# Optimization experiments

Measured on AMD Instinct MI355X. Metric: run time of the kernel, lower is better.

## Reference

```python
import jax, jax.numpy as jnp
import numpy as np

R, N, F, B = 8, 4096, 256, 16384


def setup_inputs() -> dict:
    key = jax.random.key(0)
    ks = jax.random.split(key, 9)
    adjacency = jax.random.uniform(ks[0], (R, N, N), dtype=jnp.float32)
    features = jax.random.normal(ks[1], (N, F), dtype=jnp.float32)
    c = jax.random.uniform(ks[2], (R, N, 1), dtype=jnp.float32)
    W1 = jax.random.normal(ks[3], (R, F, F), dtype=jnp.float32)
    W2 = jax.random.normal(ks[4], (R, F, F), dtype=jnp.float32)
    # DistMult relation matrices initialized as diagonal matrices (as in torch source)
    rel_mats = jax.vmap(jnp.diag)(jax.random.normal(ks[5], (R, F), dtype=jnp.float32))
    e1_idx = jax.random.randint(ks[6], (B,), 0, N, dtype=jnp.int32)
    rel_idx = jax.random.randint(ks[7], (B,), 0, R, dtype=jnp.int32)
    e2_idx = jax.random.randint(ks[8], (B,), 0, N, dtype=jnp.int32)
    return {"adjacency": adjacency, "features": features, "c": c,
            "W1": W1, "W2": W2, "rel_mats": rel_mats,
            "e1_idx": e1_idx, "rel_idx": rel_idx, "e2_idx": e2_idx}


def _rgcn_layer(A, H, c, W):
    # y = sum_r c[r] * (A[r] @ H @ W[r].T)
    AH = jnp.einsum('rnm,mf->rnf', A, H)          # [R,N,F]
    out = jnp.einsum('rnf,rof->rno', AH, W)       # [R,N,O]
    return jnp.sum(c * out, axis=0)               # [N,O]


def reference(adjacency, features, c, W1, W2, rel_mats, e1_idx, rel_idx, e2_idx):
    H = _rgcn_layer(adjacency, features, c, W1)
    H = _rgcn_layer(adjacency, H, c, W2)
    E1 = H[e1_idx]                                # [B,F]
    E2 = H[e2_idx]                                # [B,F]
    # score_b = sigmoid(E1_b @ M[rel_b] @ E2_b), computed without gathering [B,F,F]
    T = jnp.einsum('bf,rfg->brg', E1, rel_mats)   # [B,R,F]
    Tb = jnp.take_along_axis(T, rel_idx[:, None, None], axis=1)[:, 0]  # [B,F]
    return jax.nn.sigmoid(jnp.sum(Tb * E2, axis=-1))  # [B]
```

## Files before the change

kernel.cpp:

```cpp
#include <hip/hip_runtime.h>
#include <math.h>

#define NN 4096
#define FF 256
#define RR 8
#define BQ 16384

typedef _Float16 half_t;
typedef half_t v8h __attribute__((ext_vector_type(8)));
typedef float  v4f __attribute__((ext_vector_type(4)));

#define G_SCALE     0.015625f
#define G_SCALE_INV 64.0f

__global__ __launch_bounds__(256) void gemm_g(const float* __restrict__ H,
                                              const float* __restrict__ W,
                                              half_t* __restrict__ Ght,
                                              half_t* __restrict__ Glt) {
    __shared__ float smem[2 * 32 * 68];
    float (*Hs)[68] = (float(*)[68])smem;
    float (*Ws)[68] = (float(*)[68])(smem + 2176);

    const int tid = threadIdx.x;
    const int r   = blockIdx.z;
    const int o0  = blockIdx.x * 64;
    const int m0  = blockIdx.y * 64;
    const int tx  = tid & 15;
    const int ty  = tid >> 4;

    const float* __restrict__ Wr = W + (size_t)r * FF * FF;

    const int lr = tid >> 2;
    const int lc = (tid & 3) * 8;

    float acc[4][4];
#pragma unroll
    for (int i = 0; i < 4; ++i)
#pragma unroll
        for (int j = 0; j < 4; ++j) acc[i][j] = 0.0f;

    for (int fb = 0; fb < FF; fb += 32) {
        float4 h0 = *(const float4*)&H[(size_t)(m0 + lr) * FF + fb + lc];
        float4 h1 = *(const float4*)&H[(size_t)(m0 + lr) * FF + fb + lc + 4];
        float4 w0 = *(const float4*)&Wr[(size_t)(o0 + lr) * FF + fb + lc];
        float4 w1 = *(const float4*)&Wr[(size_t)(o0 + lr) * FF + fb + lc + 4];

        __syncthreads();
        Hs[lc + 0][lr] = h0.x;  Hs[lc + 1][lr] = h0.y;
        Hs[lc + 2][lr] = h0.z;  Hs[lc + 3][lr] = h0.w;
        Hs[lc + 4][lr] = h1.x;  Hs[lc + 5][lr] = h1.y;
        Hs[lc + 6][lr] = h1.z;  Hs[lc + 7][lr] = h1.w;
        Ws[lc + 0][lr] = w0.x;  Ws[lc + 1][lr] = w0.y;
        Ws[lc + 2][lr] = w0.z;  Ws[lc + 3][lr] = w0.w;
        Ws[lc + 4][lr] = w1.x;  Ws[lc + 5][lr] = w1.y;
        Ws[lc + 6][lr] = w1.z;  Ws[lc + 7][lr] = w1.w;
        __syncthreads();

#pragma unroll
        for (int k = 0; k < 32; ++k) {
            float4 hv = *(const float4*)&Hs[k][ty * 4];
            float4 wv = *(const float4*)&Ws[k][tx * 4];
            float a[4] = {hv.x, hv.y, hv.z, hv.w};
            float b[4] = {wv.x, wv.y, wv.z, wv.w};
#pragma unroll
            for (int i = 0; i < 4; ++i)
#pragma unroll
                for (int j = 0; j < 4; ++j) acc[i][j] += a[i] * b[j];
        }
    }

    __syncthreads();
    float (*T)[65] = (float(*)[65])smem;
#pragma unroll
    for (int i = 0; i < 4; ++i)
#pragma unroll
        for (int j = 0; j < 4; ++j)
            T[ty * 4 + i][tx * 4 + j] = acc[i][j] * G_SCALE;
    __syncthreads();

    const int fr = tid >> 2;
    const int mc = (tid & 3) << 4;
    v8h h0, h1, l0, l1;
#pragma unroll
    for (int q = 0; q < 8; ++q) {
        float v = T[mc + q][fr];
        half_t hh = (half_t)v;
        h0[q] = hh;
        l0[q] = (half_t)(v - (float)hh);
    }
#pragma unroll
    for (int q = 0; q < 8; ++q) {
        float v = T[mc + 8 + q][fr];
        half_t hh = (half_t)v;
        h1[q] = hh;
        l1[q] = (half_t)(v - (float)hh);
    }
    const size_t off = ((size_t)r * FF + o0 + fr) * NN + m0 + mc;
    *(v8h*)(Ght + off)     = h0;
    *(v8h*)(Ght + off + 8) = h1;
    *(v8h*)(Glt + off)     = l0;
    *(v8h*)(Glt + off + 8) = l1;
}

__global__ __launch_bounds__(256, 2) void gemm_ag(const float* __restrict__ A,
                                                  const half_t* __restrict__ Ght,
                                                  const half_t* __restrict__ Glt,
                                                  const float* __restrict__ c,
                                                  float* __restrict__ P) {
    __shared__ half_t Ah[128][40];
    __shared__ half_t Al[128][40];
    __shared__ half_t Bh[128][40];
    __shared__ half_t Bl[128][40];

    const int tid = threadIdx.x;
    const int r   = blockIdx.z;
    const int f0  = blockIdx.x * 128;
    const int m0  = blockIdx.y * 128;

    const float*  __restrict__ Ar  = A   + (size_t)r * NN * NN;
    const half_t* __restrict__ BhG = Ght + ((size_t)r * FF + f0) * NN;
    const half_t* __restrict__ BlG = Glt + ((size_t)r * FF + f0) * NN;

    const int srow  = tid >> 1;
    const int skoff = (tid & 1) * 16;

    const int wid  = tid >> 6;
    const int lane = tid & 63;
    const int wr   = wid >> 1;
    const int wc   = wid & 1;
    const int lrow = lane & 15;
    const int lk   = (lane >> 4) * 8;

    v4f acc[4][4];
#pragma unroll
    for (int m = 0; m < 4; ++m)
#pragma unroll
        for (int n = 0; n < 4; ++n) acc[m][n] = (v4f){0.f, 0.f, 0.f, 0.f};

    const float*  Arow  = Ar  + (size_t)(m0 + srow) * NN;
    const half_t* Bhrow = BhG + (size_t)srow * NN;
    const half_t* Blrow = BlG + (size_t)srow * NN;

    float4 pa0 = *(const float4*)(Arow + skoff);
    float4 pa1 = *(const float4*)(Arow + skoff + 4);
    float4 pa2 = *(const float4*)(Arow + skoff + 8);
    float4 pa3 = *(const float4*)(Arow + skoff + 12);
    float4 pbh0 = *(const float4*)(Bhrow + skoff);
    float4 pbh1 = *(const float4*)(Bhrow + skoff + 8);
    float4 pbl0 = *(const float4*)(Blrow + skoff);
    float4 pbl1 = *(const float4*)(Blrow + skoff + 8);

    for (int kb = 0; kb < NN; kb += 32) {
        __syncthreads();
        {
            float av[16];
            *(float4*)(av + 0)  = pa0;
            *(float4*)(av + 4)  = pa1;
            *(float4*)(av + 8)  = pa2;
            *(float4*)(av + 12) = pa3;
            v8h h0, h1, l0, l1;
#pragma unroll
            for (int e = 0; e < 8; ++e) {
                half_t hh = (half_t)av[e];
                h0[e] = hh;
                l0[e] = (half_t)(av[e] - (float)hh);
            }
#pragma unroll
            for (int e = 0; e < 8; ++e) {
                half_t hh = (half_t)av[8 + e];
                h1[e] = hh;
                l1[e] = (half_t)(av[8 + e] - (float)hh);
            }
            *(v8h*)&Ah[srow][skoff]     = h0;
            *(v8h*)&Ah[srow][skoff + 8] = h1;
            *(v8h*)&Al[srow][skoff]     = l0;
            *(v8h*)&Al[srow][skoff + 8] = l1;
            *(float4*)&Bh[srow][skoff]     = pbh0;
            *(float4*)&Bh[srow][skoff + 8] = pbh1;
            *(float4*)&Bl[srow][skoff]     = pbl0;
            *(float4*)&Bl[srow][skoff + 8] = pbl1;
        }
        __syncthreads();

        if (kb + 32 < NN) {
            const int kn = kb + 32;
            pa0 = *(const float4*)(Arow + kn + skoff);
            pa1 = *(const float4*)(Arow + kn + skoff + 4);
            pa2 = *(const float4*)(Arow + kn + skoff + 8);
            pa3 = *(const float4*)(Arow + kn + skoff + 12);
            pbh0 = *(const float4*)(Bhrow + kn + skoff);
            pbh1 = *(const float4*)(Bhrow + kn + skoff + 8);
            pbl0 = *(const float4*)(Blrow + kn + skoff);
            pbl1 = *(const float4*)(Blrow + kn + skoff + 8);
        }

        v8h bh[4], bl[4];
#pragma unroll
        for (int n = 0; n < 4; ++n) {
            const int bc = wc * 64 + n * 16 + lrow;
            bh[n] = *(const v8h*)&Bh[bc][lk];
            bl[n] = *(const v8h*)&Bl[bc][lk];
        }
#pragma unroll
        for (int m = 0; m < 4; ++m) {
            const int ar = wr * 64 + m * 16 + lrow;
            v8h ahf = *(const v8h*)&Ah[ar][lk];
            v8h alf = *(const v8h*)&Al[ar][lk];
#pragma unroll
            for (int n = 0; n < 4; ++n) {
                acc[m][n] = __builtin_amdgcn_mfma_f32_16x16x32_f16(alf, bh[n], acc[m][n], 0, 0, 0);
                acc[m][n] = __builtin_amdgcn_mfma_f32_16x16x32_f16(ahf, bl[n], acc[m][n], 0, 0, 0);
                acc[m][n] = __builtin_amdgcn_mfma_f32_16x16x32_f16(ahf, bh[n], acc[m][n], 0, 0, 0);
            }
        }
    }

    float* __restrict__ Pp = P + (size_t)r * NN * FF;
#pragma unroll
    for (int m = 0; m < 4; ++m) {
        const int gm0 = m0 + wr * 64 + m * 16 + ((lane >> 4) << 2);
        float cv[4];
#pragma unroll
        for (int j = 0; j < 4; ++j)
            cv[j] = c[r * NN + gm0 + j] * G_SCALE_INV;
#pragma unroll
        for (int n = 0; n < 4; ++n) {
            const int gf = f0 + wc * 64 + n * 16 + (lane & 15);
#pragma unroll
            for (int j = 0; j < 4; ++j)
                Pp[(size_t)(gm0 + j) * FF + gf] = acc[m][n][j] * cv[j];
        }
    }
}

__global__ __launch_bounds__(256) void reduce_p(const float* __restrict__ P,
                                                float* __restrict__ Hout) {
    const size_t idx = ((size_t)blockIdx.x * 256 + threadIdx.x) * 4;
    float4 s = *(const float4*)&P[idx];
#pragma unroll
    for (int r = 1; r < RR; ++r) {
        float4 v = *(const float4*)&P[(size_t)r * NN * FF + idx];
        s.x += v.x; s.y += v.y; s.z += v.z; s.w += v.w;
    }
    *(float4*)&Hout[idx] = s;
}

__global__ __launch_bounds__(256) void score_k(const float* __restrict__ H2,
                                               const float* __restrict__ relm,
                                               const int* __restrict__ e1,
                                               const int* __restrict__ rel,
                                               const int* __restrict__ e2,
                                               float* __restrict__ out) {
    const int wave = threadIdx.x >> 6;
    const int lane = threadIdx.x & 63;
    const int b = blockIdx.x * 4 + wave;
    if (b >= BQ) return;

    const int rr = rel[b];
    const float4* __restrict__ x = (const float4*)(H2 + (size_t)e1[b] * FF);
    const float4* __restrict__ y = (const float4*)(H2 + (size_t)e2[b] * FF);
    const float* __restrict__ M = relm + (size_t)rr * FF * FF;

    float4 xv = x[lane];
    float4 yv = y[lane];
    const int f = lane * 4;
    float s = xv.x * yv.x * M[(size_t)(f + 0) * (FF + 1)]
            + xv.y * yv.y * M[(size_t)(f + 1) * (FF + 1)]
            + xv.z * yv.z * M[(size_t)(f + 2) * (FF + 1)]
            + xv.w * yv.w * M[(size_t)(f + 3) * (FF + 1)];

#pragma unroll
    for (int off = 32; off > 0; off >>= 1) s += __shfl_down(s, off, 64);

    if (lane == 0) out[b] = 1.0f / (1.0f + expf(-s));
}

extern "C" void kernel_launch(void* const* d_in, const int* in_sizes, int n_in,
                              void* d_out, int out_size, void* d_ws, size_t ws_size,
                              hipStream_t stream) {
    const float* A    = (const float*)d_in[0];
    const float* feat = (const float*)d_in[1];
    const float* c    = (const float*)d_in[2];
    const float* W1   = (const float*)d_in[3];
    const float* W2   = (const float*)d_in[4];
    const float* relm = (const float*)d_in[5];
    const int*   e1   = (const int*)d_in[6];
    const int*   rel  = (const int*)d_in[7];
    const int*   e2   = (const int*)d_in[8];
    float* out = (float*)d_out;

    const size_t GT = (size_t)RR * FF * NN;
    half_t* Ght = (half_t*)d_ws;
    half_t* Glt = Ght + GT;
    float*  P   = (float*)(Glt + GT);
    float*  H   = P + (size_t)RR * NN * FF;

    dim3 gg(FF / 64, NN / 64, RR);
    dim3 ga(FF / 128, NN / 128, RR);
    const int gr = (NN * FF / 4) / 256;

    gemm_g  <<<gg, 256, 0, stream>>>(feat, W1, Ght, Glt);
    gemm_ag <<<ga, 256, 0, stream>>>(A, Ght, Glt, c, P);
    reduce_p<<<gr, 256, 0, stream>>>(P, H);
    gemm_g  <<<gg, 256, 0, stream>>>(H, W2, Ght, Glt);
    gemm_ag <<<ga, 256, 0, stream>>>(A, Ght, Glt, c, P);
    reduce_p<<<gr, 256, 0, stream>>>(P, H);
    score_k<<<BQ / 4, 256, 0, stream>>>(H, relm, e1, rel, e2, out);
}
```

Before: 1.231 ms.

## Pre-split adjacency into fp16 hi/lo once and split-K the aggregation GEMM

```diff
diff --git a/kernel.cpp b/kernel.cpp
--- a/kernel.cpp
+++ b/kernel.cpp
@@ -102,15 +102,141 @@
     *(v8h*)(Glt + off + 8) = l1;
 }
 
+__global__ __launch_bounds__(256) void split_a(const float* __restrict__ A,
+                                               half_t* __restrict__ Ah,
+                                               half_t* __restrict__ Al) {
+    const size_t total  = (size_t)RR * NN * NN / 8;
+    const size_t stride = (size_t)gridDim.x * 256;
+    for (size_t g = (size_t)blockIdx.x * 256 + threadIdx.x; g < total; g += stride) {
+        const float* src = A + g * 8;
+        float4 f0 = *(const float4*)(src);
+        float4 f1 = *(const float4*)(src + 4);
+        float av[8] = {f0.x, f0.y, f0.z, f0.w, f1.x, f1.y, f1.z, f1.w};
+        v8h h, l;
+#pragma unroll
+        for (int e = 0; e < 8; ++e) {
+            half_t hh = (half_t)av[e];
+            h[e] = hh;
+            l[e] = (half_t)(av[e] - (float)hh);
+        }
+        *(v8h*)(Ah + g * 8) = h;
+        *(v8h*)(Al + g * 8) = l;
+    }
+}
+
+__global__ __launch_bounds__(256, 3) void gemm_ag_fast(const half_t* __restrict__ Ah,
+                                                       const half_t* __restrict__ Al,
+                                                       const half_t* __restrict__ Ght,
+                                                       const half_t* __restrict__ Glt,
+                                                       const float* __restrict__ c,
+                                                       float* __restrict__ P) {
+    __shared__ half_t S[4][128][40];
+
+    const int tid = threadIdx.x;
+    const int bid = blockIdx.x;
+    const int r   = bid & 7;
+    const int pos = bid >> 3;
+    const int fb  = pos & 1;
+    const int kh  = (pos >> 1) & 1;
+    const int mb  = pos >> 2;
+    const int m0  = mb * 128;
+    const int f0  = fb * 128;
+    const int k0  = kh * (NN / 2);
+
+    const int srow  = tid >> 1;
+    const int skoff = (tid & 1) * 16;
+
+    const half_t* __restrict__ g0 = Ah  + ((size_t)r * NN + m0 + srow) * NN + k0 + skoff;
+    const half_t* __restrict__ g1 = Al  + ((size_t)r * NN + m0 + srow) * NN + k0 + skoff;
+    const half_t* __restrict__ g2 = Ght + ((size_t)r * FF + f0 + srow) * NN + k0 + skoff;
+    const half_t* __restrict__ g3 = Glt + ((size_t)r * FF + f0 + srow) * NN + k0 + skoff;
+
+    const int wid  = tid >> 6;
+    const int lane = tid & 63;
+    const int wr   = wid >> 1;
+    const int wc   = wid & 1;
+    const int lrow = lane & 15;
+    const int lk8  = (lane >> 4) * 8;
+
+    v4f acc[4][4];
+#pragma unroll
+    for (int m = 0; m < 4; ++m)
+#pragma unroll
+        for (int n = 0; n < 4; ++n) acc[m][n] = (v4f){0.f, 0.f, 0.f, 0.f};
+
+    v8h p00 = *(const v8h*)(g0);     v8h p01 = *(const v8h*)(g0 + 8);
+    v8h p10 = *(const v8h*)(g1);     v8h p11 = *(const v8h*)(g1 + 8);
+    v8h p20 = *(const v8h*)(g2);     v8h p21 = *(const v8h*)(g2 + 8);
+    v8h p30 = *(const v8h*)(g3);     v8h p31 = *(const v8h*)(g3 + 8);
+
+    for (int kb = 0; kb < NN / 2; kb += 32) {
+        __syncthreads();
+        *(v8h*)&S[0][srow][skoff]     = p00;
+        *(v8h*)&S[0][srow][skoff + 8] = p01;
+        *(v8h*)&S[1][srow][skoff]     = p10;
+        *(v8h*)&S[1][srow][skoff + 8] = p11;
+        *(v8h*)&S[2][srow][skoff]     = p20;
+        *(v8h*)&S[2][srow][skoff + 8] = p21;
+        *(v8h*)&S[3][srow][skoff]     = p30;
+        *(v8h*)&S[3][srow][skoff + 8] = p31;
+        __syncthreads();
+
+        if (kb + 32 < NN / 2) {
+            const int kn = kb + 32;
+            p00 = *(const v8h*)(g0 + kn);     p01 = *(const v8h*)(g0 + kn + 8);
+            p10 = *(const v8h*)(g1 + kn);     p11 = *(const v8h*)(g1 + kn + 8);
+            p20 = *(const v8h*)(g2 + kn);     p21 = *(const v8h*)(g2 + kn + 8);
+            p30 = *(const v8h*)(g3 + kn);     p31 = *(const v8h*)(g3 + kn + 8);
+        }
+
+        v8h bh[4], bl[4];
+#pragma unroll
+        for (int n = 0; n < 4; ++n) {
+            const int bc = wc * 64 + n * 16 + lrow;
+            bh[n] = *(const v8h*)&S[2][bc][lk8];
+            bl[n] = *(const v8h*)&S[3][bc][lk8];
+        }
+#pragma unroll
+        for (int m = 0; m < 4; ++m) {
+            const int ar = wr * 64 + m * 16 + lrow;
+            v8h ahf = *(const v8h*)&S[0][ar][lk8];
+            v8h alf = *(const v8h*)&S[1][ar][lk8];
+#pragma unroll
+            for (int n = 0; n < 4; ++n) {
+                acc[m][n] = __builtin_amdgcn_mfma_f32_16x16x32_f16(alf, bh[n], acc[m][n], 0, 0, 0);
+                acc[m][n] = __builtin_amdgcn_mfma_f32_16x16x32_f16(ahf, bl[n], acc[m][n], 0, 0, 0);
+                acc[m][n] = __builtin_amdgcn_mfma_f32_16x16x32_f16(ahf, bh[n], acc[m][n], 0, 0, 0);
+            }
+        }
+    }
+
+    float* __restrict__ Pp = P + (size_t)(r * 2 + kh) * NN * FF;
+#pragma unroll
+    for (int m = 0; m < 4; ++m) {
+        const int gm0 = m0 + wr * 64 + m * 16 + ((lane >> 4) << 2);
+        float cv[4];
+#pragma unroll
+        for (int j = 0; j < 4; ++j)
+            cv[j] = c[r * NN + gm0 + j] * G_SCALE_INV;
+#pragma unroll
+        for (int n = 0; n < 4; ++n) {
+            const int gf = f0 + wc * 64 + n * 16 + (lane & 15);
+#pragma unroll
+            for (int j = 0; j < 4; ++j)
+                Pp[(size_t)(gm0 + j) * FF + gf] = acc[m][n][j] * cv[j];
+        }
+    }
+}
+
 __global__ __launch_bounds__(256, 2) void gemm_ag(const float* __restrict__ A,
                                                   const half_t* __restrict__ Ght,
                                                   const half_t* __restrict__ Glt,
                                                   const float* __restrict__ c,
                                                   float* __restrict__ P) {
-    __shared__ half_t Ah[128][40];
-    __shared__ half_t Al[128][40];
-    __shared__ half_t Bh[128][40];
-    __shared__ half_t Bl[128][40];
+    __shared__ half_t Ahs[128][40];
+    __shared__ half_t Als[128][40];
+    __shared__ half_t Bhs[128][40];
+    __shared__ half_t Bls[128][40];
 
     const int tid = threadIdx.x;
     const int r   = blockIdx.z;
@@ -171,14 +297,14 @@
                 h1[e] = hh;
                 l1[e] = (half_t)(av[8 + e] - (float)hh);
             }
-            *(v8h*)&Ah[srow][skoff]     = h0;
-            *(v8h*)&Ah[srow][skoff + 8] = h1;
-            *(v8h*)&Al[srow][skoff]     = l0;
-            *(v8h*)&Al[srow][skoff + 8] = l1;
-            *(float4*)&Bh[srow][skoff]     = pbh0;
-            *(float4*)&Bh[srow][skoff + 8] = pbh1;
-            *(float4*)&Bl[srow][skoff]     = pbl0;
-            *(float4*)&Bl[srow][skoff + 8] = pbl1;
+            *(v8h*)&Ahs[srow][skoff]     = h0;
+            *(v8h*)&Ahs[srow][skoff + 8] = h1;
+            *(v8h*)&Als[srow][skoff]     = l0;
+            *(v8h*)&Als[srow][skoff + 8] = l1;
+            *(float4*)&Bhs[srow][skoff]     = pbh0;
+            *(float4*)&Bhs[srow][skoff + 8] = pbh1;
+            *(float4*)&Bls[srow][skoff]     = pbl0;
+            *(float4*)&Bls[srow][skoff + 8] = pbl1;
         }
         __syncthreads();
 
@@ -198,14 +324,14 @@
 #pragma unroll
         for (int n = 0; n < 4; ++n) {
             const int bc = wc * 64 + n * 16 + lrow;
-            bh[n] = *(const v8h*)&Bh[bc][lk];
-            bl[n] = *(const v8h*)&Bl[bc][lk];
+            bh[n] = *(const v8h*)&Bhs[bc][lk];
+            bl[n] = *(const v8h*)&Bls[bc][lk];
         }
 #pragma unroll
         for (int m = 0; m < 4; ++m) {
             const int ar = wr * 64 + m * 16 + lrow;
-            v8h ahf = *(const v8h*)&Ah[ar][lk];
-            v8h alf = *(const v8h*)&Al[ar][lk];
+            v8h ahf = *(const v8h*)&Ahs[ar][lk];
+            v8h alf = *(const v8h*)&Als[ar][lk];
 #pragma unroll
             for (int n = 0; n < 4; ++n) {
                 acc[m][n] = __builtin_amdgcn_mfma_f32_16x16x32_f16(alf, bh[n], acc[m][n], 0, 0, 0);
@@ -234,11 +360,11 @@
 }
 
 __global__ __launch_bounds__(256) void reduce_p(const float* __restrict__ P,
-                                                float* __restrict__ Hout) {
+                                                float* __restrict__ Hout,
+                                                int np) {
     const size_t idx = ((size_t)blockIdx.x * 256 + threadIdx.x) * 4;
     float4 s = *(const float4*)&P[idx];
-#pragma unroll
-    for (int r = 1; r < RR; ++r) {
+    for (int r = 1; r < np; ++r) {
         float4 v = *(const float4*)&P[(size_t)r * NN * FF + idx];
         s.x += v.x; s.y += v.y; s.z += v.z; s.w += v.w;
     }
@@ -289,21 +415,45 @@
     const int*   e2   = (const int*)d_in[8];
     float* out = (float*)d_out;
 
-    const size_t GT = (size_t)RR * FF * NN;
-    half_t* Ght = (half_t*)d_ws;
-    half_t* Glt = Ght + GT;
-    float*  P   = (float*)(Glt + GT);
-    float*  H   = P + (size_t)RR * NN * FF;
+    const size_t GTh   = (size_t)RR * FF * NN;
+    const size_t AEls  = (size_t)RR * NN * NN;
+    const size_t fast_need = AEls * 2 * sizeof(half_t)
+                           + GTh * 2 * sizeof(half_t)
+                           + (size_t)16 * NN * FF * sizeof(float)
+                           + (size_t)NN * FF * sizeof(float);
 
     dim3 gg(FF / 64, NN / 64, RR);
-    dim3 ga(FF / 128, NN / 128, RR);
     const int gr = (NN * FF / 4) / 256;
 
-    gemm_g  <<<gg, 256, 0, stream>>>(feat, W1, Ght, Glt);
-    gemm_ag <<<ga, 256, 0, stream>>>(A, Ght, Glt, c, P);
-    reduce_p<<<gr, 256, 0, stream>>>(P, H);
-    gemm_g  <<<gg, 256, 0, stream>>>(H, W2, Ght, Glt);
-    gemm_ag <<<ga, 256, 0, stream>>>(A, Ght, Glt, c, P);
-    reduce_p<<<gr, 256, 0, stream>>>(P, H);
-    score_k<<<BQ / 4, 256, 0, stream>>>(H, relm, e1, rel, e2, out);
-}
+    if (ws_size >= fast_need) {
+        half_t* Ah  = (half_t*)d_ws;
+        half_t* Al  = Ah + AEls;
+        half_t* Ght = Al + AEls;
+        half_t* Glt = Ght + GTh;
+        float*  P   = (float*)(Glt + GTh);
+        float*  H   = P + (size_t)16 * NN * FF;
+
+        split_a<<<2048, 256, 0, stream>>>(A, Ah, Al);
+        gemm_g      <<<gg, 256, 0, stream>>>(feat, W1, Ght, Glt);
+        gemm_ag_fast<<<1024, 256, 0, stream>>>(Ah, Al, Ght, Glt, c, P);
+        reduce_p    <<<gr, 256, 0, stream>>>(P, H, 16);
+        gemm_g      <<<gg, 256, 0, stream>>>(H, W2, Ght, Glt);
+        gemm_ag_fast<<<1024, 256, 0, stream>>>(Ah, Al, Ght, Glt, c, P);
+        reduce_p    <<<gr, 256, 0, stream>>>(P, H, 16);
+        score_k<<<BQ / 4, 256, 0, stream>>>(H, relm, e1, rel, e2, out);
+    } else {
+        half_t* Ght = (half_t*)d_ws;
+        half_t* Glt = Ght + GTh;
+        float*  P   = (float*)(Glt + GTh);
+        float*  H   = P + (size_t)RR * NN * FF;
+
+        dim3 ga(FF / 128, NN / 128, RR);
+        gemm_g <<<gg, 256, 0, stream>>>(feat, W1, Ght, Glt);
+        gemm_ag<<<ga, 256, 0, stream>>>(A, Ght, Glt, c, P);
+        reduce_p<<<gr, 256, 0, stream>>>(P, H, RR);
+        gemm_g <<<gg, 256, 0, stream>>>(H, W2, Ght, Glt);
+        gemm_ag<<<ga, 256, 0, stream>>>(A, Ght, Glt, c, P);
+        reduce_p<<<gr, 256, 0, stream>>>(P, H, RR);
+        score_k<<<BQ / 4, 256, 0, stream>>>(H, relm, e1, rel, e2, out);
+    }
+}
```

Measured after the change: 1.441 ms. 1.17x slower.
